# Performance work log

Measured on AMD Instinct MI355X. Metric: run time of the kernel, lower is better.

The kernel has to match this reference:

```python
import jax, jax.numpy as jnp
import numpy as np

DECISIVE_CONFIDENCE = 0.5
LOG_CLAMP = -100.0  # torch binary_cross_entropy clamps log terms at -100

B, L = 4096, 8192


def setup_inputs() -> dict:
    key = jax.random.key(0)
    k1, k2, k3 = jax.random.split(key, 3)
    pred = jax.random.uniform(k1, (B, L), dtype=jnp.float32)
    truth = jax.random.randint(k2, (B, L), 0, 2).astype(jnp.float32)
    lengths = jax.random.randint(k3, (B,), 0, L, dtype=jnp.int32)
    return {"pred": pred, "truth": truth, "lengths": lengths}


def reference(pred, truth, lengths):
    b, l = pred.shape
    mask = jnp.arange(l, dtype=lengths.dtype)[None, :] < lengths[:, None]  # [B, L] valid positions

    # replace NaN/Inf in pred with 0 (matches torch.where(isnan/isinf, 0, pred))
    p = jnp.where(jnp.isfinite(pred), pred, jnp.zeros_like(pred))

    # BCE with torch-style log clamping at -100
    logp = jnp.maximum(jnp.log(p), LOG_CLAMP)
    log1mp = jnp.maximum(jnp.log1p(-p), LOG_CLAMP)
    bce = -(truth * logp + (1.0 - truth) * log1mp)
    bce = jnp.where(mask, bce, 0.0)

    len_f = lengths.astype(pred.dtype)
    # per-sequence mean BCE; empty sequences contribute 0 (continue in original)
    per_seq = jnp.where(lengths > 0, bce.sum(axis=1) / jnp.maximum(len_f, 1.0), 0.0)
    loss = per_seq.sum() / b  # divided by len(pred) = B

    pred_bin = (p > DECISIVE_CONFIDENCE) & mask
    targ_bin = (truth > 0) & mask
    gp = targ_bin.sum()
    gn = (mask & ~targ_bin).sum()
    tp = (pred_bin & targ_bin).sum()
    tn = (mask & ~pred_bin & ~targ_bin).sum()

    gp = jnp.maximum(gp, 1)
    gn = jnp.maximum(gn, 1)
    accuracy = (tp / gp) * (tn / gn)
    return loss, accuracy
```

## Files before the change

### kernel.cpp

```cpp
#include <hip/hip_runtime.h>
#include <math.h>

#define BLOCK 256

__device__ __forceinline__ float waveRedF(float v) {
#pragma unroll
    for (int o = 32; o > 0; o >>= 1) v += __shfl_down(v, o, 64);
    return v;
}
__device__ __forceinline__ unsigned waveRedU(unsigned v) {
#pragma unroll
    for (int o = 32; o > 0; o >>= 1) v += __shfl_down(v, o, 64);
    return v;
}

__device__ __forceinline__ void elem(float p, float t, float& bce,
                                     unsigned& tp, unsigned& tn,
                                     unsigned& gp, unsigned& gn) {
    p = __builtin_isfinite(p) ? p : 0.0f;
    float lp = fmaxf(__logf(p), -100.0f);
    float lq = fmaxf(__logf(1.0f - p), -100.0f);
    bce -= t * lp + (1.0f - t) * lq;
    bool tb = t > 0.0f;
    bool pb = p > 0.5f;
    gp += (unsigned)tb;
    gn += (unsigned)(!tb);
    tp += (unsigned)(pb && tb);
    tn += (unsigned)(!pb && !tb);
}

__global__ __launch_bounds__(BLOCK) void rowKernel(
    const float* __restrict__ pred, const float* __restrict__ truth,
    const int* __restrict__ lengths, int B, int L,
    float* __restrict__ lossPart, unsigned* __restrict__ cntPart) {
    const int row = blockIdx.x;
    const int len = lengths[row];

    float bce = 0.0f;
    unsigned tp = 0, tn = 0, gp = 0, gn = 0;

    if (len > 0) {
        const float* pr = pred + (size_t)row * L;
        const float* tr = truth + (size_t)row * L;
        const float4* pv = (const float4*)pr;
        const float4* tv = (const float4*)tr;
        const int nvec = len >> 2;
        for (int v = threadIdx.x; v < nvec; v += BLOCK) {
            float4 p4 = pv[v];
            float4 t4 = tv[v];
            elem(p4.x, t4.x, bce, tp, tn, gp, gn);
            elem(p4.y, t4.y, bce, tp, tn, gp, gn);
            elem(p4.z, t4.z, bce, tp, tn, gp, gn);
            elem(p4.w, t4.w, bce, tp, tn, gp, gn);
        }
        const int base = nvec << 2;
        const int tail = len - base;
        if ((int)threadIdx.x < tail) {
            float p = pr[base + threadIdx.x];
            float t = tr[base + threadIdx.x];
            elem(p, t, bce, tp, tn, gp, gn);
        }
    }

    bce = waveRedF(bce);
    tp = waveRedU(tp); tn = waveRedU(tn);
    gp = waveRedU(gp); gn = waveRedU(gn);

    __shared__ float sf[BLOCK / 64];
    __shared__ unsigned su[4][BLOCK / 64];
    const int wid = threadIdx.x >> 6;
    const int lane = threadIdx.x & 63;
    if (lane == 0) {
        sf[wid] = bce;
        su[0][wid] = tp; su[1][wid] = tn; su[2][wid] = gp; su[3][wid] = gn;
    }
    __syncthreads();
    if (threadIdx.x == 0) {
        float bsum = 0.0f;
        unsigned ctp = 0, ctn = 0, cgp = 0, cgn = 0;
#pragma unroll
        for (int w = 0; w < BLOCK / 64; w++) {
            bsum += sf[w];
            ctp += su[0][w]; ctn += su[1][w]; cgp += su[2][w]; cgn += su[3][w];
        }
        lossPart[row] = (len > 0) ? (bsum / (float)len) : 0.0f;
        cntPart[row]           = ctp;
        cntPart[B + row]       = ctn;
        cntPart[2 * B + row]   = cgp;
        cntPart[3 * B + row]   = cgn;
    }
}

__global__ __launch_bounds__(BLOCK) void finalKernel(
    const float* __restrict__ lossPart, const unsigned* __restrict__ cntPart,
    int B, float* __restrict__ out) {
    float ls = 0.0f;
    unsigned tp = 0, tn = 0, gp = 0, gn = 0;
    for (int i = threadIdx.x; i < B; i += BLOCK) {
        ls += lossPart[i];
        tp += cntPart[i];
        tn += cntPart[B + i];
        gp += cntPart[2 * B + i];
        gn += cntPart[3 * B + i];
    }
    ls = waveRedF(ls);
    tp = waveRedU(tp); tn = waveRedU(tn);
    gp = waveRedU(gp); gn = waveRedU(gn);

    __shared__ float sf[BLOCK / 64];
    __shared__ unsigned su[4][BLOCK / 64];
    const int wid = threadIdx.x >> 6;
    const int lane = threadIdx.x & 63;
    if (lane == 0) {
        sf[wid] = ls;
        su[0][wid] = tp; su[1][wid] = tn; su[2][wid] = gp; su[3][wid] = gn;
    }
    __syncthreads();
    if (threadIdx.x == 0) {
        float bsum = 0.0f;
        unsigned ctp = 0, ctn = 0, cgp = 0, cgn = 0;
#pragma unroll
        for (int w = 0; w < BLOCK / 64; w++) {
            bsum += sf[w];
            ctp += su[0][w]; ctn += su[1][w]; cgp += su[2][w]; cgn += su[3][w];
        }
        if (cgp == 0) cgp = 1;
        if (cgn == 0) cgn = 1;
        out[0] = bsum / (float)B;
        out[1] = ((float)ctp / (float)cgp) * ((float)ctn / (float)cgn);
    }
}

extern "C" void kernel_launch(void* const* d_in, const int* in_sizes, int n_in,
                              void* d_out, int out_size, void* d_ws, size_t ws_size,
                              hipStream_t stream) {
    const float* pred    = (const float*)d_in[0];
    const float* truth   = (const float*)d_in[1];
    const int*   lengths = (const int*)d_in[2];
    const int B = in_sizes[2];
    const int L = in_sizes[0] / B;

    float*    lossPart = (float*)d_ws;
    unsigned* cntPart  = (unsigned*)((char*)d_ws + (size_t)B * sizeof(float));

    rowKernel<<<B, BLOCK, 0, stream>>>(pred, truth, lengths, B, L, lossPart, cntPart);
    finalKernel<<<1, BLOCK, 0, stream>>>(lossPart, cntPart, B, (float*)d_out);
}
```

Measured before the change: 254.7 us.

## Split each row into fixed-size chunks across a 2D grid and use a single log

The per-row kernel becomes a chunked kernel: a 2D grid of rows by 2048-element chunks, so variable-length rows are spread across more, evenly sized blocks instead of one block per row doing all the work. The per-chunk partial sums are reduced in a final single-block kernel, which now also divides by the row length. Separately, the BCE is computed with one log of the selected probability instead of two logs. The final reduction now handles four times as many partials, and the single-log form treats truth as binary.

```diff
diff --git a/kernel.cpp b/kernel.cpp
--- a/kernel.cpp
+++ b/kernel.cpp
@@ -2,6 +2,7 @@
 #include <math.h>
 
 #define BLOCK 256
+#define CHUNK 2048
 
 __device__ __forceinline__ float waveRedF(float v) {
 #pragma unroll
@@ -18,33 +19,37 @@
                                      unsigned& tp, unsigned& tn,
                                      unsigned& gp, unsigned& gn) {
     p = __builtin_isfinite(p) ? p : 0.0f;
-    float lp = fmaxf(__logf(p), -100.0f);
-    float lq = fmaxf(__logf(1.0f - p), -100.0f);
-    bce -= t * lp + (1.0f - t) * lq;
-    bool tb = t > 0.0f;
-    bool pb = p > 0.5f;
+    const bool tb = t > 0.0f;
+    const bool pb = p > 0.5f;
+    const float x = tb ? p : (1.0f - p);
+    bce -= fmaxf(__logf(x), -100.0f);
     gp += (unsigned)tb;
     gn += (unsigned)(!tb);
-    tp += (unsigned)(pb && tb);
-    tn += (unsigned)(!pb && !tb);
+    tp += (unsigned)(pb & tb);
+    tn += (unsigned)((!pb) & (!tb));
 }
 
-__global__ __launch_bounds__(BLOCK) void rowKernel(
+__global__ __launch_bounds__(BLOCK) void chunkKernel(
     const float* __restrict__ pred, const float* __restrict__ truth,
-    const int* __restrict__ lengths, int B, int L,
-    float* __restrict__ lossPart, unsigned* __restrict__ cntPart) {
-    const int row = blockIdx.x;
-    const int len = lengths[row];
+    const int* __restrict__ lengths, int L, int nchunk, int NB,
+    float* __restrict__ bceP, unsigned* __restrict__ cntP) {
+    const int row  = blockIdx.x;
+    const int c    = blockIdx.y;
+    const int slot = row * nchunk + c;
+    const int len  = lengths[row];
+    const int start = c * CHUNK;
+    const int stop  = min(len, start + CHUNK);
 
     float bce = 0.0f;
     unsigned tp = 0, tn = 0, gp = 0, gn = 0;
 
-    if (len > 0) {
-        const float* pr = pred + (size_t)row * L;
-        const float* tr = truth + (size_t)row * L;
+    if (start < stop) {
+        const float* pr = pred  + (size_t)row * L + start;
+        const float* tr = truth + (size_t)row * L + start;
+        const int n    = stop - start;
+        const int nvec = n >> 2;
         const float4* pv = (const float4*)pr;
         const float4* tv = (const float4*)tr;
-        const int nvec = len >> 2;
         for (int v = threadIdx.x; v < nvec; v += BLOCK) {
             float4 p4 = pv[v];
             float4 t4 = tv[v];
@@ -54,11 +59,9 @@
             elem(p4.w, t4.w, bce, tp, tn, gp, gn);
         }
         const int base = nvec << 2;
-        const int tail = len - base;
+        const int tail = n - base;
         if ((int)threadIdx.x < tail) {
-            float p = pr[base + threadIdx.x];
-            float t = tr[base + threadIdx.x];
-            elem(p, t, bce, tp, tn, gp, gn);
+            elem(pr[base + threadIdx.x], tr[base + threadIdx.x], bce, tp, tn, gp, gn);
         }
     }
 
@@ -68,7 +71,7 @@
 
     __shared__ float sf[BLOCK / 64];
     __shared__ unsigned su[4][BLOCK / 64];
-    const int wid = threadIdx.x >> 6;
+    const int wid  = threadIdx.x >> 6;
     const int lane = threadIdx.x & 63;
     if (lane == 0) {
         sf[wid] = bce;
@@ -83,50 +86,59 @@
             bsum += sf[w];
             ctp += su[0][w]; ctn += su[1][w]; cgp += su[2][w]; cgn += su[3][w];
         }
-        lossPart[row] = (len > 0) ? (bsum / (float)len) : 0.0f;
-        cntPart[row]           = ctp;
-        cntPart[B + row]       = ctn;
-        cntPart[2 * B + row]   = cgp;
-        cntPart[3 * B + row]   = cgn;
+        bceP[slot]          = bsum;
+        cntP[slot]          = ctp;
+        cntP[NB + slot]     = ctn;
+        cntP[2 * NB + slot] = cgp;
+        cntP[3 * NB + slot] = cgn;
     }
 }
 
-__global__ __launch_bounds__(BLOCK) void finalKernel(
-    const float* __restrict__ lossPart, const unsigned* __restrict__ cntPart,
-    int B, float* __restrict__ out) {
-    float ls = 0.0f;
+__global__ __launch_bounds__(BLOCK) void reduceKernel(
+    const float* __restrict__ bceP, const unsigned* __restrict__ cntP,
+    const int* __restrict__ lengths, int B, int nchunk, int NB,
+    float* __restrict__ out) {
+    float loss = 0.0f;
     unsigned tp = 0, tn = 0, gp = 0, gn = 0;
-    for (int i = threadIdx.x; i < B; i += BLOCK) {
-        ls += lossPart[i];
-        tp += cntPart[i];
-        tn += cntPart[B + i];
-        gp += cntPart[2 * B + i];
-        gn += cntPart[3 * B + i];
+
+    for (int r = threadIdx.x; r < B; r += BLOCK) {
+        float s = 0.0f;
+#pragma unroll 4
+        for (int c = 0; c < nchunk; c++) s += bceP[r * nchunk + c];
+        const int len = lengths[r];
+        loss += (len > 0) ? (s / (float)len) : 0.0f;
     }
-    ls = waveRedF(ls);
+    for (int i = threadIdx.x; i < NB; i += BLOCK) {
+        tp += cntP[i];
+        tn += cntP[NB + i];
+        gp += cntP[2 * NB + i];
+        gn += cntP[3 * NB + i];
+    }
+
+    loss = waveRedF(loss);
     tp = waveRedU(tp); tn = waveRedU(tn);
     gp = waveRedU(gp); gn = waveRedU(gn);
 
     __shared__ float sf[BLOCK / 64];
     __shared__ unsigned su[4][BLOCK / 64];
-    const int wid = threadIdx.x >> 6;
+    const int wid  = threadIdx.x >> 6;
     const int lane = threadIdx.x & 63;
     if (lane == 0) {
-        sf[wid] = ls;
+        sf[wid] = loss;
         su[0][wid] = tp; su[1][wid] = tn; su[2][wid] = gp; su[3][wid] = gn;
     }
     __syncthreads();
     if (threadIdx.x == 0) {
-        float bsum = 0.0f;
+        float lsum = 0.0f;
         unsigned ctp = 0, ctn = 0, cgp = 0, cgn = 0;
 #pragma unroll
         for (int w = 0; w < BLOCK / 64; w++) {
-            bsum += sf[w];
+            lsum += sf[w];
             ctp += su[0][w]; ctn += su[1][w]; cgp += su[2][w]; cgn += su[3][w];
         }
         if (cgp == 0) cgp = 1;
         if (cgn == 0) cgn = 1;
-        out[0] = bsum / (float)B;
+        out[0] = lsum / (float)B;
         out[1] = ((float)ctp / (float)cgp) * ((float)ctn / (float)cgn);
     }
 }
@@ -139,10 +151,13 @@
     const int*   lengths = (const int*)d_in[2];
     const int B = in_sizes[2];
     const int L = in_sizes[0] / B;
+    const int nchunk = (L + CHUNK - 1) / CHUNK;
+    const int NB = B * nchunk;
 
-    float*    lossPart = (float*)d_ws;
-    unsigned* cntPart  = (unsigned*)((char*)d_ws + (size_t)B * sizeof(float));
+    float*    bceP = (float*)d_ws;
+    unsigned* cntP = (unsigned*)((char*)d_ws + (size_t)NB * sizeof(float));
 
-    rowKernel<<<B, BLOCK, 0, stream>>>(pred, truth, lengths, B, L, lossPart, cntPart);
-    finalKernel<<<1, BLOCK, 0, stream>>>(lossPart, cntPart, B, (float*)d_out);
+    dim3 grid(B, nchunk);
+    chunkKernel<<<grid, BLOCK, 0, stream>>>(pred, truth, lengths, L, nchunk, NB, bceP, cntP);
+    reduceKernel<<<1, BLOCK, 0, stream>>>(bceP, cntP, lengths, B, nchunk, NB, (float*)d_out);
 }
```

Result: slower. 267.0 us (+4.8%).
